# Optimization experiments

Hardware: AMD Instinct MI355X
Metric: run time of the kernel (lower is better)

## Reference

```python
import jax, jax.numpy as jnp
import numpy as np

D = 1024        # embed_size
F = 4096        # ffn_dim
E = 8           # n_experts
K = 2           # top_k_experts
NS = 1          # n_shared
T = 8192        # tokens


def setup_inputs() -> dict:
    key = jax.random.key(0)
    ks = jax.random.split(key, 12)
    s = lambda *sh: 1.0 / np.sqrt(sh[-2] if len(sh) > 1 else sh[-1])
    inp = {
        "x": jax.random.normal(ks[0], (T, D), jnp.float32),
        "gate_w": jax.random.normal(ks[1], (D, E), jnp.float32) * (1.0 / np.sqrt(D)),
        "gate_b": jnp.zeros((E,), jnp.float32),
        "shared_w1": jax.random.normal(ks[2], (NS, D, 2 * F), jnp.float32) * (1.0 / np.sqrt(D)),
        "shared_b1": jnp.zeros((NS, 2 * F), jnp.float32),
        "shared_w2": jax.random.normal(ks[3], (NS, F, D), jnp.float32) * (1.0 / np.sqrt(F)),
        "shared_b2": jnp.zeros((NS, D), jnp.float32),
        "routed_w1": jax.random.normal(ks[4], (E, D, 2 * F), jnp.float32) * (1.0 / np.sqrt(D)),
        "routed_b1": jnp.zeros((E, 2 * F), jnp.float32),
        "routed_w2": jax.random.normal(ks[5], (E, F, D), jnp.float32) * (1.0 / np.sqrt(F)),
        "routed_b2": jnp.zeros((E, D), jnp.float32),
    }
    return inp


def _expert(x, w1, b1, w2, b2):
    # SwiGLU FFN: w2( silu(a) * b ) where [a, b] = chunk(x @ w1 + b1)
    h = x @ w1 + b1                      # [T, 2F]
    a, b = jnp.split(h, 2, axis=-1)      # [T, F] each
    return (jax.nn.silu(a) * b) @ w2 + b2  # [T, D]


def reference(x, gate_w, gate_b, shared_w1, shared_b1, shared_w2, shared_b2,
              routed_w1, routed_b1, routed_w2, routed_b2):
    # shared experts (always active)
    shared_out = jnp.zeros_like(x)
    for i in range(NS):
        shared_out = shared_out + _expert(x, shared_w1[i], shared_b1[i], shared_w2[i], shared_b2[i])

    # softmax gating + top-k selection
    logits = x @ gate_w + gate_b                      # [T, E]
    probs = jax.nn.softmax(logits, axis=-1)
    topk_probs, topk_idx = jax.lax.top_k(probs, K)    # [T, K]

    # per-token combine weight for each expert: sum_k p_k * 1[idx_k == e]
    one_hot = jax.nn.one_hot(topk_idx, E, dtype=x.dtype)        # [T, K, E]
    combine = jnp.einsum("tk,tke->te", topk_probs, one_hot)     # [T, E]

    # dispatch/combine: dense per-expert FFN, weighted by combine (zero off-route)
    routed_out = jnp.zeros_like(x)
    for e in range(E):
        y = _expert(x, routed_w1[e], routed_b1[e], routed_w2[e], routed_b2[e])
        routed_out = routed_out + y * combine[:, e:e + 1]

    return shared_out + routed_out
```

## Files before the change

### kernel.cpp

```cpp
#include <hip/hip_runtime.h>

#define TOK   8192
#define DD    1024
#define FF    4096
#define EE    8
#define TWOF  8192
#define NSLOT 16384

typedef unsigned short u16;
typedef float  f32x16 __attribute__((ext_vector_type(16)));
typedef __bf16 bf16x8 __attribute__((ext_vector_type(8)));

__device__ __forceinline__ u16 f2b(float f) {
  unsigned u = __builtin_bit_cast(unsigned, f);
  u += 0x7fffu + ((u >> 16) & 1u);
  return (u16)(u >> 16);
}

__device__ __forceinline__ void ldslds16(const void* g, void* l) {
  __builtin_amdgcn_global_load_lds((const __attribute__((address_space(1))) void*)g,
                                   (__attribute__((address_space(3))) void*)l, 16, 0, 0);
}

__device__ __forceinline__ int imin(int a, int b) { return a < b ? a : b; }

__global__ void gate_kernel(const float* __restrict__ x, const float* __restrict__ gw,
                            const float* __restrict__ gb, int* __restrict__ counts,
                            int* __restrict__ eidx, int* __restrict__ epos,
                            float* __restrict__ ew) {
  const int wave = threadIdx.x >> 6, lane = threadIdx.x & 63;
  const int t = blockIdx.x * 4 + wave;
  float acc[EE] = {0,0,0,0,0,0,0,0};
  const float* xr = x + (size_t)t * DD;
  for (int d = lane; d < DD; d += 64) {
    float xv = xr[d];
    const float* g = gw + (size_t)d * EE;
#pragma unroll
    for (int e = 0; e < EE; ++e) acc[e] += xv * g[e];
  }
#pragma unroll
  for (int e = 0; e < EE; ++e)
#pragma unroll
    for (int off = 32; off > 0; off >>= 1) acc[e] += __shfl_down(acc[e], off);
  if (lane == 0) {
    float l[EE];
#pragma unroll
    for (int e = 0; e < EE; ++e) l[e] = acc[e] + gb[e];
    int i0 = 0;
    for (int e = 1; e < EE; ++e) if (l[e] > l[i0]) i0 = e;
    int i1 = (i0 == 0) ? 1 : 0;
    for (int e = 0; e < EE; ++e) { if (e == i0) continue; if (l[e] > l[i1]) i1 = e; }
    float m = l[0];
    for (int e = 1; e < EE; ++e) m = fmaxf(m, l[e]);
    float s = 0.f, p[EE];
    for (int e = 0; e < EE; ++e) { p[e] = __expf(l[e] - m); s += p[e]; }
    float w0 = p[i0] / s, w1 = p[i1] / s;
    int p0 = atomicAdd(&counts[i0], 1);
    int p1 = atomicAdd(&counts[i1], 1);
    eidx[2*t] = i0; eidx[2*t+1] = i1;
    epos[2*t] = p0; epos[2*t+1] = p1;
    ew[2*t] = w0;  ew[2*t+1] = w1;
  }
}

__global__ void slot_kernel(const int* __restrict__ eidx, const int* __restrict__ epos,
                            const float* __restrict__ ew, const int* __restrict__ counts,
                            int* __restrict__ s2t, float* __restrict__ swt,
                            int* __restrict__ t2s) {
  int i = blockIdx.x * 256 + threadIdx.x;
  int e = eidx[i];
  int off = 0;
  for (int j = 0; j < e; ++j) off += counts[j];
  int slot = off + epos[i];
  s2t[slot] = i >> 1;
  swt[slot] = ew[i];
  t2s[i] = slot;
}

__global__ void cvtx_kernel(const float* __restrict__ x, u16* __restrict__ xb) {
  int i = blockIdx.x * 256 + threadIdx.x;
  float4 v = ((const float4*)x)[i];
  unsigned lo = (unsigned)f2b(v.x) | ((unsigned)f2b(v.y) << 16);
  unsigned hi = (unsigned)f2b(v.z) | ((unsigned)f2b(v.w) << 16);
  ((uint2*)xb)[i] = make_uint2(lo, hi);
}

__global__ void gather_kernel(const u16* __restrict__ xb, const int* __restrict__ s2t,
                              u16* __restrict__ xg) {
  int i = blockIdx.x * 256 + threadIdx.x;
  int row = i >> 7, c = i & 127;
  int tok = s2t[row];
  ((int4*)xg)[(size_t)row * 128 + c] = ((const int4*)xb)[(size_t)tok * 128 + c];
}

__global__ void wt_kernel(const float* __restrict__ srcS, const float* __restrict__ srcR,
                          u16* __restrict__ dst, int K, int N, int permute) {
  __shared__ float tile[32][33];
  const int seg = blockIdx.z;
  const float* src = (seg == 0) ? srcS : srcR + (size_t)(seg - 1) * K * N;
  const int pc0 = blockIdx.x * 32, k0 = blockIdx.y * 32;
  const int tid = threadIdx.x;
  {
    int kk = tid >> 3, j4 = (tid & 7) << 2;
    const float* srow = src + (size_t)(k0 + kk) * N;
#pragma unroll
    for (int q = 0; q < 4; ++q) {
      int n = pc0 + j4 + q;
      int oc = permute ? (((n >> 6) << 5) + (n & 31) + ((n & 32) ? FF : 0)) : n;
      tile[kk][j4 + q] = srow[oc];
    }
  }
  __syncthreads();
  {
    int pp = tid >> 3, kq = (tid & 7) << 2;
    u16* drow = dst + (size_t)seg * N * K + (size_t)(pc0 + pp) * K + k0 + kq;
#pragma unroll
    for (int q = 0; q < 4; ++q) drow[q] = f2b(tile[kq + q][pp]);
  }
}


__device__ __forceinline__ void kloop32(int niter,
    const char* a0, const char* a1, const char* a2, const char* a3,
    const char* b0, const char* b1, const char* b2, const char* b3,
    u16* As, u16* Bs, int tid, f32x16 (&acc)[2][2]) {
  const int lane = tid & 63, l31 = lane & 31, kg = (lane >> 5) * 16;
  const int wid = tid >> 6, wm = wid >> 1, wn = wid & 1;
  const int C = (l31 & 7) << 4;
  const char* rA[4]; const char* rB[4];
#pragma unroll
  for (int ks = 0; ks < 4; ++ks) {
    const int o = (ks * 32 + kg) ^ C;
    rA[ks] = (const char*)As + (wm * 64 + l31) * 128 + o;
    rB[ks] = (const char*)Bs + (wn * 64 + l31) * 128 + o;
  }
  for (int it = 0; it < niter; ++it) {
    const long long kb = (long long)it * 128;
    ldslds16(a0 + kb, As + tid * 8);
    ldslds16(a1 + kb, As + 2048 + tid * 8);
    ldslds16(a2 + kb, As + 4096 + tid * 8);
    ldslds16(a3 + kb, As + 6144 + tid * 8);
    ldslds16(b0 + kb, Bs + tid * 8);
    ldslds16(b1 + kb, Bs + 2048 + tid * 8);
    ldslds16(b2 + kb, Bs + 4096 + tid * 8);
    ldslds16(b3 + kb, Bs + 6144 + tid * 8);
    __syncthreads();
#pragma unroll
    for (int ks = 0; ks < 4; ++ks) {
      bf16x8 af0 = *(const bf16x8*)(rA[ks]);
      bf16x8 af1 = *(const bf16x8*)(rA[ks] + 4096);
      bf16x8 bq0 = *(const bf16x8*)(rB[ks]);
      bf16x8 bq1 = *(const bf16x8*)(rB[ks] + 4096);
      acc[0][0] = __builtin_amdgcn_mfma_f32_32x32x16_bf16(af0, bq0, acc[0][0], 0, 0, 0);
      acc[0][1] = __builtin_amdgcn_mfma_f32_32x32x16_bf16(af0, bq1, acc[0][1], 0, 0, 0);
      acc[1][0] = __builtin_amdgcn_mfma_f32_32x32x16_bf16(af1, bq0, acc[1][0], 0, 0, 0);
      acc[1][1] = __builtin_amdgcn_mfma_f32_32x32x16_bf16(af1, bq1, acc[1][1], 0, 0, 0);
    }
    __syncthreads();
  }
}

__global__ __launch_bounds__(256, 4)
void gemm1_kernel(const u16* __restrict__ xb, const u16* __restrict__ xg,
                  const u16* __restrict__ w1t, const float* __restrict__ sb1,
                  const float* __restrict__ rb1, const int* __restrict__ counts,
                  u16* __restrict__ hs) {
  __shared__ __align__(16) u16 As[128 * 64];
  __shared__ __align__(16) u16 Bs[128 * 64];
  const int seg = blockIdx.z;
  int rowstart, rows, hsbase, atot;
  const u16* A;
  if (seg == 0) { A = xb; rowstart = 0; rows = TOK; hsbase = 0; atot = TOK; }
  else {
    int o0 = 0;
    for (int j = 0; j < seg - 1; ++j) o0 += counts[j];
    A = xg; rowstart = o0; rows = counts[seg - 1]; hsbase = TOK + o0; atot = NSLOT;
  }
  const int tm = blockIdx.y;
  if (tm * 128 >= rows) return;
  const int tn = blockIdx.x;
  const int tid = threadIdx.x, lane = tid & 63, wid = tid >> 6;
  const int wm = wid >> 1, wn = wid & 1;

  const int srow = tid >> 3;
  const int scol = ((tid & 7) * 16) ^ ((srow & 7) << 4);
  const char* Ac = (const char*)A;
  const char* Bc = (const char*)(w1t + (size_t)seg * TWOF * DD);
  const char* a[4]; const char* b[4];
#pragma unroll
  for (int r = 0; r < 4; ++r) {
    int rg = imin(rowstart + tm * 128 + r * 32 + srow, atot - 1);
    a[r] = Ac + (size_t)rg * (DD * 2) + scol;
    b[r] = Bc + (size_t)(tn * 128 + r * 32 + srow) * (DD * 2) + scol;
  }

  f32x16 acc[2][2] = {};
  kloop32(DD / 64, a[0], a[1], a[2], a[3], b[0], b[1], b[2], b[3],
          As, Bs, tid, acc);

  const int l31 = lane & 31, lg = lane >> 5;
  const int rlim = rows - tm * 128;
  const float* b1 = (seg == 0) ? sb1 : rb1 + (size_t)(seg - 1) * TWOF;
  const int f = (tn * 2 + wn) * 32 + l31;
  const float ba = b1[f], bb = b1[FF + f];
  u16* hbase = hs + (size_t)(hsbase + tm * 128) * FF;
#pragma unroll
  for (int mi = 0; mi < 2; ++mi)
#pragma unroll
    for (int reg = 0; reg < 16; ++reg) {
      int lr = wm * 64 + mi * 32 + (reg & 3) + 8 * (reg >> 2) + 4 * lg;
      if (lr < rlim) {
        float av = acc[mi][0][reg] + ba;
        float bv = acc[mi][1][reg] + bb;
        float sv = av / (1.0f + __expf(-av)) * bv;
        hbase[(size_t)lr * FF + f] = f2b(sv);
      }
    }
}

__global__ __launch_bounds__(256, 4)
void gemm2_kernel(const u16* __restrict__ hs, const u16* __restrict__ w2t,
                  const float* __restrict__ sb2, const float* __restrict__ rb2,
                  const int* __restrict__ counts, float* __restrict__ yo) {
  __shared__ __align__(16) u16 As[128 * 64];
  __shared__ __align__(16) u16 Bs[128 * 64];
  const int seg = blockIdx.z;
  int rows, hrow0;
  if (seg == 0) { rows = TOK; hrow0 = 0; }
  else {
    int o0 = 0;
    for (int j = 0; j < seg - 1; ++j) o0 += counts[j];
    rows = counts[seg - 1]; hrow0 = TOK + o0;
  }
  const int tm = blockIdx.y;
  if (tm * 128 >= rows) return;
  const int tn = blockIdx.x;
  const int tid = threadIdx.x, lane = tid & 63, wid = tid >> 6;
  const int wm = wid >> 1, wn = wid & 1;

  const int srow = tid >> 3;
  const int scol = ((tid & 7) * 16) ^ ((srow & 7) << 4);
  const char* Ac = (const char*)hs;
  const char* Bc = (const char*)(w2t + (size_t)seg * DD * FF);
  const char* a[4]; const char* b[4];
#pragma unroll
  for (int r = 0; r < 4; ++r) {
    a[r] = Ac + (size_t)(hrow0 + tm * 128 + r * 32 + srow) * (FF * 2) + scol;
    b[r] = Bc + (size_t)(tn * 128 + r * 32 + srow) * (FF * 2) + scol;
  }

  f32x16 acc[2][2] = {};
  kloop32(FF / 64, a[0], a[1], a[2], a[3], b[0], b[1], b[2], b[3],
          As, Bs, tid, acc);

  const int l31 = lane & 31, lg = lane >> 5;
  const int rlim = rows - tm * 128;
  const float* b2 = (seg == 0) ? sb2 : rb2 + (size_t)(seg - 1) * DD;
  const int c0 = tn * 128 + wn * 64 + l31;
  const float bias0 = b2[c0], bias1 = b2[c0 + 32];
  float* ybase = yo + (size_t)(hrow0 + tm * 128) * DD;
#pragma unroll
  for (int mi = 0; mi < 2; ++mi)
#pragma unroll
    for (int reg = 0; reg < 16; ++reg) {
      int lr = wm * 64 + mi * 32 + (reg & 3) + 8 * (reg >> 2) + 4 * lg;
      if (lr < rlim) {
        float* orow = ybase + (size_t)lr * DD;
        orow[c0]      = acc[mi][0][reg] + bias0;
        orow[c0 + 32] = acc[mi][1][reg] + bias1;
      }
    }
}

__global__ void combine_kernel(const float* __restrict__ yo, const int* __restrict__ t2s,
                               const float* __restrict__ ew, float* __restrict__ out) {
  const int t = blockIdx.x, d = threadIdx.x;
  const float4 a  = ((const float4*)(yo + (size_t)t * DD))[d];
  const int s0 = t2s[2*t], s1 = t2s[2*t+1];
  const float w0 = ew[2*t], w1 = ew[2*t+1];
  const float4 r0 = ((const float4*)(yo + (size_t)(TOK + s0) * DD))[d];
  const float4 r1 = ((const float4*)(yo + (size_t)(TOK + s1) * DD))[d];
  float4 r;
  r.x = a.x + w0 * r0.x + w1 * r1.x;
  r.y = a.y + w0 * r0.y + w1 * r1.y;
  r.z = a.z + w0 * r0.z + w1 * r1.z;
  r.w = a.w + w0 * r0.w + w1 * r1.w;
  ((float4*)(out + (size_t)t * DD))[d] = r;
}

extern "C" void kernel_launch(void* const* d_in, const int* in_sizes, int n_in,
                              void* d_out, int out_size, void* d_ws, size_t ws_size,
                              hipStream_t stream) {
  const float* x   = (const float*)d_in[0];
  const float* gw  = (const float*)d_in[1];
  const float* gb  = (const float*)d_in[2];
  const float* sw1 = (const float*)d_in[3];
  const float* sb1 = (const float*)d_in[4];
  const float* sw2 = (const float*)d_in[5];
  const float* sb2 = (const float*)d_in[6];
  const float* rw1 = (const float*)d_in[7];
  const float* rb1 = (const float*)d_in[8];
  const float* rw2 = (const float*)d_in[9];
  const float* rb2 = (const float*)d_in[10];
  float* out = (float*)d_out;

  char* p = (char*)d_ws;
  auto alloc = [&](size_t bytes) { char* r = p; p += (bytes + 255) & ~(size_t)255; return r; };
  int*   counts = (int*)alloc(EE * 4);
  int*   eidx   = (int*)alloc((size_t)2 * TOK * 4);
  int*   epos   = (int*)alloc((size_t)2 * TOK * 4);
  float* ew     = (float*)alloc((size_t)2 * TOK * 4);
  int*   s2t    = (int*)alloc((size_t)NSLOT * 4);
  float* swt    = (float*)alloc((size_t)NSLOT * 4);
  int*   t2s    = (int*)alloc((size_t)2 * TOK * 4);
  u16*   xb     = (u16*)alloc((size_t)TOK * DD * 2);
  u16*   xg     = (u16*)alloc((size_t)NSLOT * DD * 2);
  u16*   w1t    = (u16*)alloc((size_t)9 * TWOF * DD * 2);
  u16*   w2t    = (u16*)alloc((size_t)9 * DD * FF * 2);
  u16*   hs     = (u16*)alloc((size_t)(TOK + NSLOT + 256) * FF * 2);
  float* yo     = (float*)w1t;

  hipMemsetAsync(counts, 0, EE * 4, stream);
  gate_kernel<<<TOK / 4, 256, 0, stream>>>(x, gw, gb, counts, eidx, epos, ew);
  slot_kernel<<<(2 * TOK) / 256, 256, 0, stream>>>(eidx, epos, ew, counts, s2t, swt, t2s);
  cvtx_kernel<<<(TOK * DD / 4) / 256, 256, 0, stream>>>(x, xb);
  gather_kernel<<<(NSLOT * 128) / 256, 256, 0, stream>>>(xb, s2t, xg);
  wt_kernel<<<dim3(TWOF / 32, DD / 32, 9), 256, 0, stream>>>(sw1, rw1, w1t, DD, TWOF, 1);
  wt_kernel<<<dim3(DD / 32, FF / 32, 9), 256, 0, stream>>>(sw2, rw2, w2t, FF, DD, 0);
  gemm1_kernel<<<dim3(TWOF / 128, 64, 9), 256, 0, stream>>>(xb, xg, w1t, sb1, rb1, counts, hs);
  gemm2_kernel<<<dim3(DD / 128, 64, 9), 256, 0, stream>>>(hs, w2t, sb2, rb2, counts, yo);
  combine_kernel<<<TOK, 256, 0, stream>>>(yo, t2s, ew, out);
}
```

Before: 1.146 ms.

## Rework expert GEMMs into 256x256 double-buffered tiles with 16x16 MFMA ping-pong

Replaces the 128x128, 4-wave GEMM loop with a shared 256x256-tile core run by 8 waves. The core uses 16x16x32 bf16 MFMAs and a double-buffered 128KB LDS stage with direct global-to-LDS loads. Prefetch of the next K slice is interleaved between MFMA groups using barriers and s_setprio. The w1 column permutation is changed to 16-wide interleaving so each wave gets matching gate/up fragments for the SwiGLU epilogue. This aims to raise arithmetic intensity and hide load latency, at the cost of one block per CU and more padded work on partial expert tiles.

```diff
diff --git a/kernel.cpp b/kernel.cpp
--- a/kernel.cpp
+++ b/kernel.cpp
@@ -8,7 +8,7 @@
 #define NSLOT 16384
 
 typedef unsigned short u16;
-typedef float  f32x16 __attribute__((ext_vector_type(16)));
+typedef float  f32x4  __attribute__((ext_vector_type(4)));
 typedef __bf16 bf16x8 __attribute__((ext_vector_type(8)));
 
 __device__ __forceinline__ u16 f2b(float f) {
@@ -22,7 +22,7 @@
                                    (__attribute__((address_space(3))) void*)l, 16, 0, 0);
 }
 
-__device__ __forceinline__ int imin(int a, int b) { return a < b ? a : b; }
+__device__ __forceinline__ long long llmin(long long a, long long b) { return a < b ? a : b; }
 
 __global__ void gate_kernel(const float* __restrict__ x, const float* __restrict__ gw,
                             const float* __restrict__ gb, int* __restrict__ counts,
@@ -106,7 +106,7 @@
 #pragma unroll
     for (int q = 0; q < 4; ++q) {
       int n = pc0 + j4 + q;
-      int oc = permute ? (((n >> 6) << 5) + (n & 31) + ((n & 32) ? FF : 0)) : n;
+      int oc = permute ? (((n >> 5) << 4) + (n & 15) + ((n & 16) ? FF : 0)) : n;
       tile[kk][j4 + q] = srow[oc];
     }
   }
@@ -120,53 +120,95 @@
 }
 
 
-__device__ __forceinline__ void kloop32(int niter,
-    const char* a0, const char* a1, const char* a2, const char* a3,
-    const char* b0, const char* b1, const char* b2, const char* b3,
-    u16* As, u16* Bs, int tid, f32x16 (&acc)[2][2]) {
-  const int lane = tid & 63, l31 = lane & 31, kg = (lane >> 5) * 16;
-  const int wid = tid >> 6, wm = wid >> 1, wn = wid & 1;
-  const int C = (l31 & 7) << 4;
-  const char* rA[4]; const char* rB[4];
-#pragma unroll
-  for (int ks = 0; ks < 4; ++ks) {
-    const int o = (ks * 32 + kg) ^ C;
-    rA[ks] = (const char*)As + (wm * 64 + l31) * 128 + o;
-    rB[ks] = (const char*)Bs + (wn * 64 + l31) * 128 + o;
-  }
-  for (int it = 0; it < niter; ++it) {
-    const long long kb = (long long)it * 128;
-    ldslds16(a0 + kb, As + tid * 8);
-    ldslds16(a1 + kb, As + 2048 + tid * 8);
-    ldslds16(a2 + kb, As + 4096 + tid * 8);
-    ldslds16(a3 + kb, As + 6144 + tid * 8);
-    ldslds16(b0 + kb, Bs + tid * 8);
-    ldslds16(b1 + kb, Bs + 2048 + tid * 8);
-    ldslds16(b2 + kb, Bs + 4096 + tid * 8);
-    ldslds16(b3 + kb, Bs + 6144 + tid * 8);
-    __syncthreads();
-#pragma unroll
-    for (int ks = 0; ks < 4; ++ks) {
-      bf16x8 af0 = *(const bf16x8*)(rA[ks]);
-      bf16x8 af1 = *(const bf16x8*)(rA[ks] + 4096);
-      bf16x8 bq0 = *(const bf16x8*)(rB[ks]);
-      bf16x8 bq1 = *(const bf16x8*)(rB[ks] + 4096);
-      acc[0][0] = __builtin_amdgcn_mfma_f32_32x32x16_bf16(af0, bq0, acc[0][0], 0, 0, 0);
-      acc[0][1] = __builtin_amdgcn_mfma_f32_32x32x16_bf16(af0, bq1, acc[0][1], 0, 0, 0);
-      acc[1][0] = __builtin_amdgcn_mfma_f32_32x32x16_bf16(af1, bq0, acc[1][0], 0, 0, 0);
-      acc[1][1] = __builtin_amdgcn_mfma_f32_32x32x16_bf16(af1, bq1, acc[1][1], 0, 0, 0);
-    }
-    __syncthreads();
-  }
-}
-
-__global__ __launch_bounds__(256, 4)
+#define MFMA16(MS, AF, BQ) \
+  _Pragma("unroll") for (int mi = 0; mi < 4; ++mi) \
+  _Pragma("unroll") for (int ni = 0; ni < 4; ++ni) \
+    acc[(MS)*4+mi][ni] = __builtin_amdgcn_mfma_f32_16x16x32_bf16(AF[mi], BQ[ni], acc[(MS)*4+mi][ni], 0, 0, 0);
+
+#define LDA4(DST, MS, KK, D) \
+  _Pragma("unroll") for (int i = 0; i < 4; ++i) \
+    DST[i] = *(const bf16x8*)(lds + (D)*32768 + afbase[(MS)*4+i] + kcol[KK]);
+
+#define LDB4(DST, KK, D) \
+  _Pragma("unroll") for (int i = 0; i < 4; ++i) \
+    DST[i] = *(const bf16x8*)(lds + (D)*32768 + bqbase[i] + kcol[KK]);
+
+#define STAGE_A(DN, KOFF) \
+  _Pragma("unroll") for (int s = 0; s < 4; ++s) \
+    ldslds16(gsA[s] + (KOFF), lds + (DN)*32768 + s*8192 + tid*16);
+
+#define STAGE_B(DN, KOFF) \
+  _Pragma("unroll") for (int s = 0; s < 4; ++s) \
+    ldslds16(gsB[s] + (KOFF), lds + 65536 + (DN)*32768 + s*8192 + tid*16);
+
+#define BAR()   __builtin_amdgcn_s_barrier()
+#define VMC0()  asm volatile("s_waitcnt vmcnt(0)" ::: "memory")
+#define PRIO(v) __builtin_amdgcn_s_setprio(v)
+
+template<int NT>
+__device__ __forceinline__ void gemm_core(
+    const char* Aseg, long long lda, long long arow0, long long armax,
+    const char* Bseg, long long ldb, long long bcol0,
+    char* lds, int tid, f32x4 (&acc)[8][4]) {
+  const int lane = tid & 63, wid = tid >> 6;
+  const int wm = wid >> 2, wn = wid & 3;
+  const int fr = lane & 15;
+  const int swz = (fr & 7) << 4;
+  int kcol[2];
+  kcol[0] = ((lane >> 4) * 16) ^ swz;
+  kcol[1] = (64 + (lane >> 4) * 16) ^ swz;
+  int afbase[8], bqbase[4];
+#pragma unroll
+  for (int mf = 0; mf < 8; ++mf) afbase[mf] = wm * 16384 + (mf * 16 + fr) * 128;
+#pragma unroll
+  for (int nf = 0; nf < 4; ++nf)
+    bqbase[nf] = 65536 + (wn >> 1) * 16384 + ((wn & 1) * 64 + nf * 16 + fr) * 128;
+
+  const int srow = tid >> 3, schunk = (tid & 7) * 16;
+  const char* gsA[4]; const char* gsB[4];
+#pragma unroll
+  for (int s = 0; s < 4; ++s) {
+    int rloc = s * 64 + srow;
+    long long rg = llmin(arow0 + rloc, armax);
+    gsA[s] = Aseg + rg * lda + (schunk ^ ((rloc & 7) << 4));
+    gsB[s] = Bseg + (bcol0 + rloc) * ldb + (schunk ^ ((rloc & 7) << 4));
+  }
+
+  bf16x8 af0[4], af1[4], bq0[4], bq1[4];
+
+  STAGE_A(0, 0); STAGE_B(0, 0);
+  VMC0(); BAR();
+  LDA4(af0, 0, 0, 0); LDB4(bq0, 0, 0);
+
+  for (int t = 0; t < NT; ++t) {
+    const int d = t & 1, dn = d ^ 1;
+    const bool more = (t + 1) < NT;
+    const long long koff = (long long)(t + 1) * 128;
+
+    LDA4(af1, 1, 0, d);
+    if (more) { STAGE_A(dn, koff); }
+    BAR(); PRIO(1); MFMA16(0, af0, bq0); PRIO(0); BAR();
+
+    LDA4(af0, 0, 1, d); LDB4(bq1, 1, d);
+    if (more) { STAGE_B(dn, koff); }
+    BAR(); PRIO(1); MFMA16(1, af1, bq0); PRIO(0); BAR();
+
+    LDA4(af1, 1, 1, d);
+    BAR(); PRIO(1); MFMA16(0, af0, bq1); PRIO(0); BAR();
+
+    if (more) { VMC0(); }
+    BAR();
+    if (more) { LDA4(af0, 0, 0, dn); LDB4(bq0, 0, dn); }
+    PRIO(1); MFMA16(1, af1, bq1); PRIO(0); BAR();
+  }
+}
+
+__global__ __launch_bounds__(512, 2)
 void gemm1_kernel(const u16* __restrict__ xb, const u16* __restrict__ xg,
                   const u16* __restrict__ w1t, const float* __restrict__ sb1,
                   const float* __restrict__ rb1, const int* __restrict__ counts,
                   u16* __restrict__ hs) {
-  __shared__ __align__(16) u16 As[128 * 64];
-  __shared__ __align__(16) u16 Bs[128 * 64];
+  __shared__ __align__(16) char lds[131072];
   const int seg = blockIdx.z;
   int rowstart, rows, hsbase, atot;
   const u16* A;
@@ -177,53 +219,44 @@
     A = xg; rowstart = o0; rows = counts[seg - 1]; hsbase = TOK + o0; atot = NSLOT;
   }
   const int tm = blockIdx.y;
-  if (tm * 128 >= rows) return;
+  if (tm * 256 >= rows) return;
   const int tn = blockIdx.x;
   const int tid = threadIdx.x, lane = tid & 63, wid = tid >> 6;
-  const int wm = wid >> 1, wn = wid & 1;
-
-  const int srow = tid >> 3;
-  const int scol = ((tid & 7) * 16) ^ ((srow & 7) << 4);
-  const char* Ac = (const char*)A;
-  const char* Bc = (const char*)(w1t + (size_t)seg * TWOF * DD);
-  const char* a[4]; const char* b[4];
-#pragma unroll
-  for (int r = 0; r < 4; ++r) {
-    int rg = imin(rowstart + tm * 128 + r * 32 + srow, atot - 1);
-    a[r] = Ac + (size_t)rg * (DD * 2) + scol;
-    b[r] = Bc + (size_t)(tn * 128 + r * 32 + srow) * (DD * 2) + scol;
-  }
-
-  f32x16 acc[2][2] = {};
-  kloop32(DD / 64, a[0], a[1], a[2], a[3], b[0], b[1], b[2], b[3],
-          As, Bs, tid, acc);
-
-  const int l31 = lane & 31, lg = lane >> 5;
-  const int rlim = rows - tm * 128;
+  const int wm = wid >> 2, wn = wid & 3;
+
+  f32x4 acc[8][4] = {};
+  gemm_core<DD / 64>((const char*)A, DD * 2, rowstart + tm * 256, atot - 1,
+                     (const char*)(w1t + (size_t)seg * TWOF * DD), DD * 2, tn * 256,
+                     lds, tid, acc);
+
+  const int fr = lane & 15, lq = lane >> 4;
+  const int rlim = rows - tm * 256;
   const float* b1 = (seg == 0) ? sb1 : rb1 + (size_t)(seg - 1) * TWOF;
-  const int f = (tn * 2 + wn) * 32 + l31;
-  const float ba = b1[f], bb = b1[FF + f];
-  u16* hbase = hs + (size_t)(hsbase + tm * 128) * FF;
-#pragma unroll
-  for (int mi = 0; mi < 2; ++mi)
-#pragma unroll
-    for (int reg = 0; reg < 16; ++reg) {
-      int lr = wm * 64 + mi * 32 + (reg & 3) + 8 * (reg >> 2) + 4 * lg;
-      if (lr < rlim) {
-        float av = acc[mi][0][reg] + ba;
-        float bv = acc[mi][1][reg] + bb;
-        float sv = av / (1.0f + __expf(-av)) * bv;
-        hbase[(size_t)lr * FF + f] = f2b(sv);
+  u16* hbase = hs + (size_t)(hsbase + tm * 256) * FF;
+#pragma unroll
+  for (int u = 0; u < 2; ++u) {
+    const int pc = (tn * 8 + wn * 2 + u) * 16 + fr;
+    const float ba = b1[pc], bb = b1[FF + pc];
+#pragma unroll
+    for (int mf = 0; mf < 8; ++mf)
+#pragma unroll
+      for (int q = 0; q < 4; ++q) {
+        int lr = wm * 128 + mf * 16 + lq * 4 + q;
+        if (lr < rlim) {
+          float av = acc[mf][2*u][q] + ba;
+          float bv = acc[mf][2*u+1][q] + bb;
+          float sv = av / (1.0f + __expf(-av)) * bv;
+          hbase[(size_t)lr * FF + pc] = f2b(sv);
+        }
       }
-    }
-}
-
-__global__ __launch_bounds__(256, 4)
+  }
+}
+
+__global__ __launch_bounds__(512, 2)
 void gemm2_kernel(const u16* __restrict__ hs, const u16* __restrict__ w2t,
                   const float* __restrict__ sb2, const float* __restrict__ rb2,
                   const int* __restrict__ counts, float* __restrict__ yo) {
-  __shared__ __align__(16) u16 As[128 * 64];
-  __shared__ __align__(16) u16 Bs[128 * 64];
+  __shared__ __align__(16) char lds[131072];
   const int seg = blockIdx.z;
   int rows, hrow0;
   if (seg == 0) { rows = TOK; hrow0 = 0; }
@@ -233,43 +266,32 @@
     rows = counts[seg - 1]; hrow0 = TOK + o0;
   }
   const int tm = blockIdx.y;
-  if (tm * 128 >= rows) return;
+  if (tm * 256 >= rows) return;
   const int tn = blockIdx.x;
   const int tid = threadIdx.x, lane = tid & 63, wid = tid >> 6;
-  const int wm = wid >> 1, wn = wid & 1;
-
-  const int srow = tid >> 3;
-  const int scol = ((tid & 7) * 16) ^ ((srow & 7) << 4);
-  const char* Ac = (const char*)hs;
-  const char* Bc = (const char*)(w2t + (size_t)seg * DD * FF);
-  const char* a[4]; const char* b[4];
-#pragma unroll
-  for (int r = 0; r < 4; ++r) {
-    a[r] = Ac + (size_t)(hrow0 + tm * 128 + r * 32 + srow) * (FF * 2) + scol;
-    b[r] = Bc + (size_t)(tn * 128 + r * 32 + srow) * (FF * 2) + scol;
-  }
-
-  f32x16 acc[2][2] = {};
-  kloop32(FF / 64, a[0], a[1], a[2], a[3], b[0], b[1], b[2], b[3],
-          As, Bs, tid, acc);
-
-  const int l31 = lane & 31, lg = lane >> 5;
-  const int rlim = rows - tm * 128;
+  const int wm = wid >> 2, wn = wid & 3;
+
+  f32x4 acc[8][4] = {};
+  gemm_core<FF / 64>((const char*)hs, FF * 2, hrow0 + tm * 256, TOK + NSLOT + 255,
+                     (const char*)(w2t + (size_t)seg * DD * FF), FF * 2, tn * 256,
+                     lds, tid, acc);
+
+  const int fr = lane & 15, lq = lane >> 4;
+  const int rlim = rows - tm * 256;
   const float* b2 = (seg == 0) ? sb2 : rb2 + (size_t)(seg - 1) * DD;
-  const int c0 = tn * 128 + wn * 64 + l31;
-  const float bias0 = b2[c0], bias1 = b2[c0 + 32];
-  float* ybase = yo + (size_t)(hrow0 + tm * 128) * DD;
-#pragma unroll
-  for (int mi = 0; mi < 2; ++mi)
-#pragma unroll
-    for (int reg = 0; reg < 16; ++reg) {
-      int lr = wm * 64 + mi * 32 + (reg & 3) + 8 * (reg >> 2) + 4 * lg;
-      if (lr < rlim) {
-        float* orow = ybase + (size_t)lr * DD;
-        orow[c0]      = acc[mi][0][reg] + bias0;
-        orow[c0 + 32] = acc[mi][1][reg] + bias1;
+  float* ybase = yo + (size_t)(hrow0 + tm * 256) * DD;
+#pragma unroll
+  for (int nf = 0; nf < 4; ++nf) {
+    const int c = tn * 256 + wn * 64 + nf * 16 + fr;
+    const float bias = b2[c];
+#pragma unroll
+    for (int mf = 0; mf < 8; ++mf)
+#pragma unroll
+      for (int q = 0; q < 4; ++q) {
+        int lr = wm * 128 + mf * 16 + lq * 4 + q;
+        if (lr < rlim) ybase[(size_t)lr * DD + c] = acc[mf][nf][q] + bias;
       }
-    }
+  }
 }
 
 __global__ void combine_kernel(const float* __restrict__ yo, const int* __restrict__ t2s,
@@ -327,7 +349,7 @@
   gather_kernel<<<(NSLOT * 128) / 256, 256, 0, stream>>>(xb, s2t, xg);
   wt_kernel<<<dim3(TWOF / 32, DD / 32, 9), 256, 0, stream>>>(sw1, rw1, w1t, DD, TWOF, 1);
   wt_kernel<<<dim3(DD / 32, FF / 32, 9), 256, 0, stream>>>(sw2, rw2, w2t, FF, DD, 0);
-  gemm1_kernel<<<dim3(TWOF / 128, 64, 9), 256, 0, stream>>>(xb, xg, w1t, sb1, rb1, counts, hs);
-  gemm2_kernel<<<dim3(DD / 128, 64, 9), 256, 0, stream>>>(hs, w2t, sb2, rb2, counts, yo);
+  gemm1_kernel<<<dim3(TWOF / 256, 64, 9), 512, 0, stream>>>(xb, xg, w1t, sb1, rb1, counts, hs);
+  gemm2_kernel<<<dim3(DD / 256, 64, 9), 512, 0, stream>>>(hs, w2t, sb2, rb2, counts, yo);
   combine_kernel<<<TOK, 256, 0, stream>>>(yo, t2s, ew, out);
 }
```

Measured after the change: 1.275 ms. +11.3%, slower.

## Compact MoE GEMM grids via padded per-expert tile map and swizzled block order

Applied to the files above, without the earlier changes.

A setup kernel computes expert offsets padded to multiples of 128 rows together with cumulative tile counts. The two GEMMs then launch a flat grid of 199 row-tile groups instead of a 64x9 grid that was mostly early-exiting blocks, mapping each block to a segment and tile through a small search. gemm1 also swizzles the tn order so consecutive blocks share A tiles, and the row clamp is dropped because the padding keeps reads in bounds. This removes the cost of launching and retiring empty blocks and may improve L2 reuse, in exchange for an extra tiny launch, a memset of s2t, and padded rows being computed.

```diff
diff --git a/kernel.cpp b/kernel.cpp
--- a/kernel.cpp
+++ b/kernel.cpp
@@ -6,6 +6,7 @@
 #define EE    8
 #define TWOF  8192
 #define NSLOT 16384
+#define PADT  17408
 
 typedef unsigned short u16;
 typedef float  f32x16 __attribute__((ext_vector_type(16)));
@@ -21,8 +22,6 @@
   __builtin_amdgcn_global_load_lds((const __attribute__((address_space(1))) void*)g,
                                    (__attribute__((address_space(3))) void*)l, 16, 0, 0);
 }
-
-__device__ __forceinline__ int imin(int a, int b) { return a < b ? a : b; }
 
 __global__ void gate_kernel(const float* __restrict__ x, const float* __restrict__ gw,
                             const float* __restrict__ gb, int* __restrict__ counts,
@@ -63,15 +62,26 @@
   }
 }
 
+__global__ void setup_kernel(const int* __restrict__ counts, int* __restrict__ meta) {
+  if (threadIdx.x == 0 && blockIdx.x == 0) {
+    int s = 0, tm = 0;
+    for (int e = 0; e < EE; ++e) {
+      meta[e] = s;
+      meta[8 + e] = tm;
+      s  += (counts[e] + 127) & ~127;
+      tm += (counts[e] + 127) >> 7;
+    }
+    meta[16] = tm;
+  }
+}
+
 __global__ void slot_kernel(const int* __restrict__ eidx, const int* __restrict__ epos,
-                            const float* __restrict__ ew, const int* __restrict__ counts,
+                            const float* __restrict__ ew, const int* __restrict__ meta,
                             int* __restrict__ s2t, float* __restrict__ swt,
                             int* __restrict__ t2s) {
   int i = blockIdx.x * 256 + threadIdx.x;
   int e = eidx[i];
-  int off = 0;
-  for (int j = 0; j < e; ++j) off += counts[j];
-  int slot = off + epos[i];
+  int slot = meta[e] + epos[i];
   s2t[slot] = i >> 1;
   swt[slot] = ew[i];
   t2s[i] = slot;
@@ -160,25 +170,33 @@
   }
 }
 
+__device__ __forceinline__ bool seg_map(int g, const int* __restrict__ counts,
+                                        const int* __restrict__ meta,
+                                        int& seg, int& tm, int& rowstart, int& rows) {
+  if (g < 64) { seg = 0; tm = g; rowstart = 0; rows = TOK; return true; }
+  int gr = g - 64;
+  if (gr >= meta[16]) return false;
+  int e = 0;
+  while (gr >= meta[8 + e + 1]) ++e;
+  seg = e + 1; tm = gr - meta[8 + e];
+  rowstart = meta[e]; rows = counts[e];
+  return true;
+}
+
 __global__ __launch_bounds__(256, 4)
 void gemm1_kernel(const u16* __restrict__ xb, const u16* __restrict__ xg,
                   const u16* __restrict__ w1t, const float* __restrict__ sb1,
                   const float* __restrict__ rb1, const int* __restrict__ counts,
-                  u16* __restrict__ hs) {
+                  const int* __restrict__ meta, u16* __restrict__ hs) {
   __shared__ __align__(16) u16 As[128 * 64];
   __shared__ __align__(16) u16 Bs[128 * 64];
-  const int seg = blockIdx.z;
-  int rowstart, rows, hsbase, atot;
-  const u16* A;
-  if (seg == 0) { A = xb; rowstart = 0; rows = TOK; hsbase = 0; atot = TOK; }
-  else {
-    int o0 = 0;
-    for (int j = 0; j < seg - 1; ++j) o0 += counts[j];
-    A = xg; rowstart = o0; rows = counts[seg - 1]; hsbase = TOK + o0; atot = NSLOT;
-  }
-  const int tm = blockIdx.y;
-  if (tm * 128 >= rows) return;
-  const int tn = blockIdx.x;
+  const int lin = blockIdx.x + 64 * blockIdx.y;
+  const int tn = (lin & 7) * 8 + ((lin >> 3) & 7);
+  const int g = lin >> 6;
+  int seg, tm, rowstart, rows;
+  if (!seg_map(g, counts, meta, seg, tm, rowstart, rows)) return;
+  const u16* A = (seg == 0) ? xb : xg;
+  const int hsbase = (seg == 0) ? 0 : TOK + rowstart;
   const int tid = threadIdx.x, lane = tid & 63, wid = tid >> 6;
   const int wm = wid >> 1, wn = wid & 1;
 
@@ -189,7 +207,7 @@
   const char* a[4]; const char* b[4];
 #pragma unroll
   for (int r = 0; r < 4; ++r) {
-    int rg = imin(rowstart + tm * 128 + r * 32 + srow, atot - 1);
+    int rg = rowstart + tm * 128 + r * 32 + srow;
     a[r] = Ac + (size_t)rg * (DD * 2) + scol;
     b[r] = Bc + (size_t)(tn * 128 + r * 32 + srow) * (DD * 2) + scol;
   }
@@ -221,20 +239,15 @@
 __global__ __launch_bounds__(256, 4)
 void gemm2_kernel(const u16* __restrict__ hs, const u16* __restrict__ w2t,
                   const float* __restrict__ sb2, const float* __restrict__ rb2,
-                  const int* __restrict__ counts, float* __restrict__ yo) {
+                  const int* __restrict__ counts, const int* __restrict__ meta,
+                  float* __restrict__ yo) {
   __shared__ __align__(16) u16 As[128 * 64];
   __shared__ __align__(16) u16 Bs[128 * 64];
-  const int seg = blockIdx.z;
-  int rows, hrow0;
-  if (seg == 0) { rows = TOK; hrow0 = 0; }
-  else {
-    int o0 = 0;
-    for (int j = 0; j < seg - 1; ++j) o0 += counts[j];
-    rows = counts[seg - 1]; hrow0 = TOK + o0;
-  }
-  const int tm = blockIdx.y;
-  if (tm * 128 >= rows) return;
   const int tn = blockIdx.x;
+  const int g = blockIdx.y;
+  int seg, tm, rowstart, rows;
+  if (!seg_map(g, counts, meta, seg, tm, rowstart, rows)) return;
+  const int hrow0 = (seg == 0) ? 0 : TOK + rowstart;
   const int tid = threadIdx.x, lane = tid & 63, wid = tid >> 6;
   const int wm = wid >> 1, wn = wid & 1;
 
@@ -307,27 +320,30 @@
   char* p = (char*)d_ws;
   auto alloc = [&](size_t bytes) { char* r = p; p += (bytes + 255) & ~(size_t)255; return r; };
   int*   counts = (int*)alloc(EE * 4);
+  int*   meta   = (int*)alloc(17 * 4);
   int*   eidx   = (int*)alloc((size_t)2 * TOK * 4);
   int*   epos   = (int*)alloc((size_t)2 * TOK * 4);
   float* ew     = (float*)alloc((size_t)2 * TOK * 4);
-  int*   s2t    = (int*)alloc((size_t)NSLOT * 4);
-  float* swt    = (float*)alloc((size_t)NSLOT * 4);
+  int*   s2t    = (int*)alloc((size_t)PADT * 4);
+  float* swt    = (float*)alloc((size_t)PADT * 4);
   int*   t2s    = (int*)alloc((size_t)2 * TOK * 4);
   u16*   xb     = (u16*)alloc((size_t)TOK * DD * 2);
-  u16*   xg     = (u16*)alloc((size_t)NSLOT * DD * 2);
+  u16*   xg     = (u16*)alloc((size_t)PADT * DD * 2);
   u16*   w1t    = (u16*)alloc((size_t)9 * TWOF * DD * 2);
   u16*   w2t    = (u16*)alloc((size_t)9 * DD * FF * 2);
-  u16*   hs     = (u16*)alloc((size_t)(TOK + NSLOT + 256) * FF * 2);
+  u16*   hs     = (u16*)alloc((size_t)(TOK + PADT + 128) * FF * 2);
   float* yo     = (float*)w1t;
 
   hipMemsetAsync(counts, 0, EE * 4, stream);
+  hipMemsetAsync(s2t, 0, (size_t)PADT * 4, stream);
   gate_kernel<<<TOK / 4, 256, 0, stream>>>(x, gw, gb, counts, eidx, epos, ew);
-  slot_kernel<<<(2 * TOK) / 256, 256, 0, stream>>>(eidx, epos, ew, counts, s2t, swt, t2s);
+  setup_kernel<<<1, 64, 0, stream>>>(counts, meta);
+  slot_kernel<<<(2 * TOK) / 256, 256, 0, stream>>>(eidx, epos, ew, meta, s2t, swt, t2s);
   cvtx_kernel<<<(TOK * DD / 4) / 256, 256, 0, stream>>>(x, xb);
-  gather_kernel<<<(NSLOT * 128) / 256, 256, 0, stream>>>(xb, s2t, xg);
+  gather_kernel<<<PADT / 2, 256, 0, stream>>>(xb, s2t, xg);
   wt_kernel<<<dim3(TWOF / 32, DD / 32, 9), 256, 0, stream>>>(sw1, rw1, w1t, DD, TWOF, 1);
   wt_kernel<<<dim3(DD / 32, FF / 32, 9), 256, 0, stream>>>(sw2, rw2, w2t, FF, DD, 0);
-  gemm1_kernel<<<dim3(TWOF / 128, 64, 9), 256, 0, stream>>>(xb, xg, w1t, sb1, rb1, counts, hs);
-  gemm2_kernel<<<dim3(DD / 128, 64, 9), 256, 0, stream>>>(hs, w2t, sb2, rb2, counts, yo);
+  gemm1_kernel<<<dim3(64, 199), 256, 0, stream>>>(xb, xg, w1t, sb1, rb1, counts, meta, hs);
+  gemm2_kernel<<<dim3(8, 199), 256, 0, stream>>>(hs, w2t, sb2, rb2, counts, meta, yo);
   combine_kernel<<<TOK, 256, 0, stream>>>(yo, t2s, ew, out);
 }
```

New measurement: 1.112 ms. 2.9% less time.
